# Kernel tuning notes

Hardware: AMD Instinct MI355X
Metric: run time of the kernel (lower is better)

## Reference

```python
import jax, jax.numpy as jnp
import numpy as np


def setup_inputs() -> dict:
    key = jax.random.key(0)
    ks = jax.random.split(key, 9)
    B, S, H, W = 4, 4096, 16, 16
    D = 256  # input_size == H*W == d_model
    sc = 1.0 / np.sqrt(D)
    return {
        "x": jax.random.normal(ks[0], (B, S, H, W), dtype=jnp.float32),
        "Wq": jax.random.normal(ks[1], (D, D), dtype=jnp.float32) * sc,
        "bq": jax.random.normal(ks[2], (D,), dtype=jnp.float32) * 0.01,
        "Wk": jax.random.normal(ks[3], (D, D), dtype=jnp.float32) * sc,
        "bk": jax.random.normal(ks[4], (D,), dtype=jnp.float32) * 0.01,
        "Wv": jax.random.normal(ks[5], (D, D), dtype=jnp.float32) * sc,
        "bv": jax.random.normal(ks[6], (D,), dtype=jnp.float32) * 0.01,
        "Wo": jax.random.normal(ks[7], (D, D), dtype=jnp.float32) * sc,
        "bo": jax.random.normal(ks[8], (D,), dtype=jnp.float32) * 0.01,
    }


def reference(x, Wq, bq, Wk, bk, Wv, bv, Wo, bo):
    B, S, H, W = x.shape
    xf = x.reshape(B, S, H * W)                      # [B, S, input_size]
    # nn.Linear: y = x @ W^T + b, weight shape [out, in]
    q = jax.nn.softplus(xf @ Wq.T + bq)              # [B, S, d]
    k = jax.nn.softplus(xf @ Wk.T + bk)              # [B, S, d]
    v = xf @ Wv.T + bv                               # [B, S, d]
    # naive ordering as in original: [B,S,S] scores, no softmax/normalization
    weight = jnp.einsum('bcd,bhd->bch', q, k)        # [B, S, S]
    result = jnp.einsum('bch,bhd->bcd', weight, v)   # [B, S, d]
    out = result @ Wo.T + bo                         # [B, S, input_size]
    return out.reshape(B, S, H, W)
```

## Files before the change

### kernel.cpp

```cpp
#include <hip/hip_runtime.h>
#include <hip/hip_bf16.h>
#include <math.h>

typedef __bf16 bf16_t;
typedef __bf16 bf16x8 __attribute__((ext_vector_type(8)));
typedef __bf16 bf16x4 __attribute__((ext_vector_type(4)));
typedef float  f32x4  __attribute__((ext_vector_type(4)));

#define NBATCH 4
#define SB     4096
#define BS     (NBATCH*SB)
#define DIM    256
#define NCHUNK 16


__device__ __forceinline__ float softplus_f(float x) {
  return fmaxf(x, 0.0f) + log1pf(__expf(-fabsf(x)));
}

__device__ __forceinline__ void gload_lds16(const void* g, void* l) {
  __builtin_amdgcn_global_load_lds(
      (const __attribute__((address_space(1))) void*)g,
      (__attribute__((address_space(3))) void*)l,
      16, 0, 0);
}

__device__ __forceinline__ void cvt4(const float* __restrict__ s,
                                     bf16_t* __restrict__ d, int qi) {
  const float4 v = *(const float4*)(s + (size_t)qi * 4);
  bf16x4 o;
  o[0] = (bf16_t)v.x; o[1] = (bf16_t)v.y; o[2] = (bf16_t)v.z; o[3] = (bf16_t)v.w;
  *(bf16x4*)(d + (size_t)qi * 4) = o;
}

__global__ void prep_all(const float* __restrict__ x,
                         const float* __restrict__ Wq,
                         const float* __restrict__ Wk,
                         const float* __restrict__ Wv,
                         const float* __restrict__ Wo,
                         const float* __restrict__ bv,
                         bf16_t* __restrict__ xb,
                         bf16_t* __restrict__ Wqb,
                         bf16_t* __restrict__ Wkb,
                         bf16_t* __restrict__ Wvob,
                         float* __restrict__ bvo) {
  if (blockIdx.x < 1024) {
    const int QX = BS * DIM / 4;
    const int QW = DIM * DIM / 4;
    const int total = QX + 2 * QW;
    for (int qi = blockIdx.x * blockDim.x + threadIdx.x; qi < total;
         qi += 1024 * blockDim.x) {
      if (qi < QX)           cvt4(x,  xb,  qi);
      else if (qi < QX + QW) cvt4(Wq, Wqb, qi - QX);
      else                   cvt4(Wk, Wkb, qi - QX - QW);
    }
  } else {
    const int j = blockIdx.x - 1024;
    const int t = threadIdx.x;
    float acc = 0.0f;
    for (int i = 0; i < DIM; ++i)
      acc = fmaf(Wo[j * DIM + i], Wv[i * DIM + t], acc);
    Wvob[(size_t)j * DIM + t] = (bf16_t)acc;
    if (t == 0) {
      float a = 0.0f;
      for (int i = 0; i < DIM; ++i) a = fmaf(Wo[j * DIM + i], bv[i], a);
      bvo[j] = a;
    }
  }
}

__device__ __forceinline__ void gemm128_core(
    const bf16_t* __restrict__ Abase,
    const bf16_t* __restrict__ Bbase,
    char* smem, int tid, f32x4 acc[4][4]) {
  const int lane = tid & 63;
  const int w = tid >> 6;
  const int wr = w & 1, wc = w >> 1;
  #pragma unroll
  for (int kk = 0; kk < 2; ++kk) {
    const char* asrc = (const char*)Abase + kk * 256;
    const char* bsrc = (const char*)Bbase + kk * 256;
    #pragma unroll
    for (int it = 0; it < 8; ++it) {
      const int L = it * 256 + tid;
      const int row = L >> 4;
      const int lch = (L & 15) ^ (row & 7);
      char* la = smem + (size_t)(it * 256 + w * 64) * 16;
      char* lb = la + 32768;
      gload_lds16(asrc + (size_t)row * 512 + lch * 16, la);
      gload_lds16(bsrc + (size_t)row * 512 + lch * 16, lb);
    }
    __syncthreads();
    #pragma unroll
    for (int ks = 0; ks < 4; ++ks) {
      const int kb = ks * 64 + ((lane >> 4) << 4);
      bf16x8 af[4], bg[4];
      #pragma unroll
      for (int mi = 0; mi < 4; ++mi) {
        const int row = wr * 64 + mi * 16 + (lane & 15);
        const int ch = (kb >> 4) ^ (row & 7);
        af[mi] = *(const bf16x8*)(smem + (size_t)row * 256 + ch * 16);
      }
      #pragma unroll
      for (int ni = 0; ni < 4; ++ni) {
        const int row = wc * 64 + ni * 16 + (lane & 15);
        const int ch = (kb >> 4) ^ (row & 7);
        bg[ni] = *(const bf16x8*)(smem + 32768 + (size_t)row * 256 + ch * 16);
      }
      #pragma unroll
      for (int mi = 0; mi < 4; ++mi)
        #pragma unroll
        for (int ni = 0; ni < 4; ++ni)
          acc[mi][ni] = __builtin_amdgcn_mfma_f32_16x16x32_bf16(
              af[mi], bg[ni], acc[mi][ni], 0, 0, 0);
    }
    __syncthreads();
  }
}

__global__ __launch_bounds__(256) void qkv_gemm(
    const bf16_t* __restrict__ xb,
    const bf16_t* __restrict__ Wqb,
    const bf16_t* __restrict__ Wkb,
    const bf16_t* __restrict__ Wvob,
    const float* __restrict__ bq,
    const float* __restrict__ bk,
    const float* __restrict__ bvo,
    bf16_t* __restrict__ qo,
    bf16_t* __restrict__ kT,
    bf16_t* __restrict__ vT) {
  __shared__ __align__(16) char smem[65536];
  const int mode = blockIdx.z;
  const int r0 = blockIdx.x * 128;
  const int c0 = blockIdx.y * 128;
  const bf16_t* W   = (mode == 0) ? Wqb : (mode == 1) ? Wkb : Wvob;
  const float* bias = (mode == 0) ? bq  : (mode == 1) ? bk  : bvo;
  const int tid = threadIdx.x;
  const int lane = tid & 63;
  const int w = tid >> 6;
  const int wr = w & 1, wc = w >> 1;

  f32x4 zero = {0.0f, 0.0f, 0.0f, 0.0f};
  f32x4 acc[4][4];
  #pragma unroll
  for (int i = 0; i < 4; ++i)
    #pragma unroll
    for (int j = 0; j < 4; ++j) acc[i][j] = zero;

  gemm128_core(xb + (size_t)r0 * DIM, W + (size_t)c0 * DIM, smem, tid, acc);

  const int batch = r0 >> 12;
  #pragma unroll
  for (int ni = 0; ni < 4; ++ni) {
    const int col = c0 + wc * 64 + ni * 16 + (lane & 15);
    const float bb = bias[col];
    #pragma unroll
    for (int mi = 0; mi < 4; ++mi) {
      const int srow = r0 + wr * 64 + mi * 16 + ((lane >> 4) << 2);
      f32x4 v = acc[mi][ni];
      float o0 = v[0] + bb, o1 = v[1] + bb, o2 = v[2] + bb, o3 = v[3] + bb;
      if (mode < 2) {
        o0 = softplus_f(o0); o1 = softplus_f(o1);
        o2 = softplus_f(o2); o3 = softplus_f(o3);
      }
      if (mode == 0) {
        qo[(size_t)(srow + 0) * DIM + col] = (bf16_t)o0;
        qo[(size_t)(srow + 1) * DIM + col] = (bf16_t)o1;
        qo[(size_t)(srow + 2) * DIM + col] = (bf16_t)o2;
        qo[(size_t)(srow + 3) * DIM + col] = (bf16_t)o3;
      } else {
        bf16_t* dst = (mode == 1) ? kT : vT;
        const int sin = srow & (SB - 1);
        bf16x4 p;
        p[0] = (bf16_t)o0; p[1] = (bf16_t)o1; p[2] = (bf16_t)o2; p[3] = (bf16_t)o3;
        *(bf16x4*)(dst + (size_t)batch * DIM * SB + (size_t)col * SB + sin) = p;
      }
    }
  }
}

__global__ __launch_bounds__(256) void m_gemm(
    const bf16_t* __restrict__ kT,
    const bf16_t* __restrict__ vT,
    float* __restrict__ MTp) {
  const int quad = blockIdx.x;
  const int sc   = blockIdx.y;
  const int b    = blockIdx.z;
  const int tid = threadIdx.x;
  const int lane = tid & 63;
  const int w = tid >> 6;
  const int wr = w & 1, wc = w >> 1;
  const int j0 = (quad & 1) * 128 + wr * 64;
  const int d0 = (quad >> 1) * 128 + wc * 64;
  const bf16_t* vb = vT + (size_t)b * DIM * SB;
  const bf16_t* kb = kT + (size_t)b * DIM * SB;

  f32x4 zero = {0.0f, 0.0f, 0.0f, 0.0f};
  f32x4 acc[4][4];
  #pragma unroll
  for (int i = 0; i < 4; ++i)
    #pragma unroll
    for (int j = 0; j < 4; ++j) acc[i][j] = zero;

  const int svec = sc * 256 + ((lane >> 4) << 3);
  #pragma unroll
  for (int it = 0; it < 8; ++it) {
    const int s = svec + it * 32;
    bf16x8 af[4], bg[4];
    #pragma unroll
    for (int mi = 0; mi < 4; ++mi)
      af[mi] = *(const bf16x8*)(vb + (size_t)(j0 + mi * 16 + (lane & 15)) * SB + s);
    #pragma unroll
    for (int ni = 0; ni < 4; ++ni)
      bg[ni] = *(const bf16x8*)(kb + (size_t)(d0 + ni * 16 + (lane & 15)) * SB + s);
    #pragma unroll
    for (int mi = 0; mi < 4; ++mi)
      #pragma unroll
      for (int ni = 0; ni < 4; ++ni)
        acc[mi][ni] = __builtin_amdgcn_mfma_f32_16x16x32_bf16(
            af[mi], bg[ni], acc[mi][ni], 0, 0, 0);
  }

  float* o = MTp + ((size_t)sc * NBATCH + b) * DIM * DIM;
  #pragma unroll
  for (int mi = 0; mi < 4; ++mi) {
    const int row = j0 + mi * 16 + ((lane >> 4) << 2);
    #pragma unroll
    for (int ni = 0; ni < 4; ++ni) {
      const int col = d0 + ni * 16 + (lane & 15);
      #pragma unroll
      for (int r = 0; r < 4; ++r)
        o[(size_t)(row + r) * DIM + col] = acc[mi][ni][r];
    }
  }
}

__global__ void reduce_nt(const float* __restrict__ MTp,
                          bf16_t* __restrict__ NTb) {
  const int qi = blockIdx.x * blockDim.x + threadIdx.x;
  f32x4 s = {0.0f, 0.0f, 0.0f, 0.0f};
  #pragma unroll
  for (int c = 0; c < NCHUNK; ++c) {
    const float4 v =
        *(const float4*)(MTp + (size_t)c * NBATCH * DIM * DIM + (size_t)qi * 4);
    s[0] += v.x; s[1] += v.y; s[2] += v.z; s[3] += v.w;
  }
  bf16x4 o;
  o[0] = (bf16_t)s[0]; o[1] = (bf16_t)s[1];
  o[2] = (bf16_t)s[2]; o[3] = (bf16_t)s[3];
  *(bf16x4*)(NTb + (size_t)qi * 4) = o;
}

__global__ __launch_bounds__(256) void out_gemm(
    const bf16_t* __restrict__ qo,
    const bf16_t* __restrict__ NTb,
    const float* __restrict__ bo,
    float* __restrict__ out) {
  __shared__ __align__(16) char smem[65536];
  const int r0 = blockIdx.x * 128;
  const int c0 = blockIdx.y * 128;
  const int batch = r0 >> 12;
  const int tid = threadIdx.x;
  const int lane = tid & 63;
  const int w = tid >> 6;
  const int wr = w & 1, wc = w >> 1;

  f32x4 zero = {0.0f, 0.0f, 0.0f, 0.0f};
  f32x4 acc[4][4];
  #pragma unroll
  for (int i = 0; i < 4; ++i)
    #pragma unroll
    for (int j = 0; j < 4; ++j) acc[i][j] = zero;

  gemm128_core(qo + (size_t)r0 * DIM,
               NTb + (size_t)batch * DIM * DIM + (size_t)c0 * DIM,
               smem, tid, acc);

  #pragma unroll
  for (int ni = 0; ni < 4; ++ni) {
    const int col = c0 + wc * 64 + ni * 16 + (lane & 15);
    const float bb = bo[col];
    #pragma unroll
    for (int mi = 0; mi < 4; ++mi) {
      const int srow = r0 + wr * 64 + mi * 16 + ((lane >> 4) << 2);
      f32x4 v = acc[mi][ni];
      #pragma unroll
      for (int r = 0; r < 4; ++r)
        out[(size_t)(srow + r) * DIM + col] = v[r] + bb;
    }
  }
}


extern "C" void kernel_launch(void* const* d_in, const int* in_sizes, int n_in,
                              void* d_out, int out_size, void* d_ws, size_t ws_size,
                              hipStream_t stream) {
  const float* x  = (const float*)d_in[0];
  const float* Wq = (const float*)d_in[1];
  const float* bq = (const float*)d_in[2];
  const float* Wk = (const float*)d_in[3];
  const float* bk = (const float*)d_in[4];
  const float* Wv = (const float*)d_in[5];
  const float* bv = (const float*)d_in[6];
  const float* Wo = (const float*)d_in[7];
  const float* bo = (const float*)d_in[8];
  float* out = (float*)d_out;

  char* ws = (char*)d_ws;
  bf16_t* xb   = (bf16_t*)(ws);
  bf16_t* qo   = (bf16_t*)(ws + 8388608);
  bf16_t* kT   = (bf16_t*)(ws + 16777216);
  bf16_t* vT   = (bf16_t*)(ws + 25165824);
  bf16_t* Wqb  = (bf16_t*)(ws + 33554432);
  bf16_t* Wkb  = (bf16_t*)(ws + 33685504);
  bf16_t* Wvob = (bf16_t*)(ws + 33816576);
  float*  bvo  = (float*)(ws + 33947648);
  bf16_t* NTb  = (bf16_t*)(ws + 33948672);
  float*  MTp  = (float*)(ws + 34472960);

  prep_all<<<1280, 256, 0, stream>>>(x, Wq, Wk, Wv, Wo, bv,
                                     xb, Wqb, Wkb, Wvob, bvo);
  qkv_gemm<<<dim3(128, 2, 3), 256, 0, stream>>>(xb, Wqb, Wkb, Wvob,
                                                bq, bk, bvo, qo, kT, vT);
  m_gemm<<<dim3(4, NCHUNK, 4), 256, 0, stream>>>(kT, vT, MTp);
  reduce_nt<<<256, 256, 0, stream>>>(MTp, NTb);
  out_gemm<<<dim3(128, 2), 256, 0, stream>>>(qo, NTb, bo, out);
}
```

Measured before the change: 149.6 us.

## Stage full weight panel in LDS and read activations directly from global

Replaces the two-step LDS-staged GEMM core with one that loads the whole 128x256 weight panel into LDS in a single step, with one barrier. The activation operand (x or q) is now read straight from global memory into registers for each MFMA step instead of going through LDS. This removes one LDS round-trip and several barriers per block. The cost is uncoalesced-ish 16-byte global loads of activations with no reuse across the two wave columns, and global latency sitting directly in the MFMA loop. The grid is also flattened from 3D to 2D so the mode index comes from blockIdx.y.

Result: slower. 175.3 us (+17.2%).

```diff
diff --git a/kernel.cpp b/kernel.cpp
--- a/kernel.cpp
+++ b/kernel.cpp
@@ -69,56 +69,54 @@
   }
 }
 
-__device__ __forceinline__ void gemm128_core(
-    const bf16_t* __restrict__ Abase,
-    const bf16_t* __restrict__ Bbase,
-    char* smem, int tid, f32x4 acc[4][4]) {
+
+__device__ __forceinline__ void stage_panel(const bf16_t* __restrict__ P,
+                                            char* smem, int tid) {
+  const int w = tid >> 6;
+  const char* src = (const char*)P;
+  #pragma unroll
+  for (int it = 0; it < 16; ++it) {
+    const int L = it * 256 + tid;
+    const int prow = L >> 5;
+    const int sch = (L & 31) ^ (prow & 7);
+    gload_lds16(src + (size_t)prow * 512 + sch * 16,
+                smem + (size_t)(it * 256 + w * 64) * 16);
+  }
+  __syncthreads();
+}
+
+__device__ __forceinline__ void panel_gemm_compute(
+    const bf16_t* __restrict__ Arow0,
+    const char* smem, int tid, f32x4 acc[4][4]) {
   const int lane = tid & 63;
   const int w = tid >> 6;
   const int wr = w & 1, wc = w >> 1;
-  #pragma unroll
-  for (int kk = 0; kk < 2; ++kk) {
-    const char* asrc = (const char*)Abase + kk * 256;
-    const char* bsrc = (const char*)Bbase + kk * 256;
-    #pragma unroll
-    for (int it = 0; it < 8; ++it) {
-      const int L = it * 256 + tid;
-      const int row = L >> 4;
-      const int lch = (L & 15) ^ (row & 7);
-      char* la = smem + (size_t)(it * 256 + w * 64) * 16;
-      char* lb = la + 32768;
-      gload_lds16(asrc + (size_t)row * 512 + lch * 16, la);
-      gload_lds16(bsrc + (size_t)row * 512 + lch * 16, lb);
-    }
-    __syncthreads();
-    #pragma unroll
-    for (int ks = 0; ks < 4; ++ks) {
-      const int kb = ks * 64 + ((lane >> 4) << 4);
-      bf16x8 af[4], bg[4];
+  const int arow_off = wr * 64 + (lane & 15);
+  const int brow_off = wc * 64 + (lane & 15);
+  const int kvec = (lane >> 4) << 3;
+  #pragma unroll
+  for (int ks = 0; ks < 8; ++ks) {
+    const int k = ks * 32 + kvec;
+    bf16x8 af[4], bg[4];
+    #pragma unroll
+    for (int mi = 0; mi < 4; ++mi)
+      af[mi] = *(const bf16x8*)(Arow0 + (size_t)(arow_off + mi * 16) * 256 + k);
+    #pragma unroll
+    for (int ni = 0; ni < 4; ++ni) {
+      const int prow = brow_off + ni * 16;
+      const int ch = (k >> 3) ^ (prow & 7);
+      bg[ni] = *(const bf16x8*)(smem + (size_t)prow * 512 + ch * 16);
+    }
+    #pragma unroll
+    for (int mi = 0; mi < 4; ++mi)
       #pragma unroll
-      for (int mi = 0; mi < 4; ++mi) {
-        const int row = wr * 64 + mi * 16 + (lane & 15);
-        const int ch = (kb >> 4) ^ (row & 7);
-        af[mi] = *(const bf16x8*)(smem + (size_t)row * 256 + ch * 16);
-      }
-      #pragma unroll
-      for (int ni = 0; ni < 4; ++ni) {
-        const int row = wc * 64 + ni * 16 + (lane & 15);
-        const int ch = (kb >> 4) ^ (row & 7);
-        bg[ni] = *(const bf16x8*)(smem + 32768 + (size_t)row * 256 + ch * 16);
-      }
-      #pragma unroll
-      for (int mi = 0; mi < 4; ++mi)
-        #pragma unroll
-        for (int ni = 0; ni < 4; ++ni)
-          acc[mi][ni] = __builtin_amdgcn_mfma_f32_16x16x32_bf16(
-              af[mi], bg[ni], acc[mi][ni], 0, 0, 0);
-    }
-    __syncthreads();
-  }
-}
-
-__global__ __launch_bounds__(256) void qkv_gemm(
+      for (int ni = 0; ni < 4; ++ni)
+        acc[mi][ni] = __builtin_amdgcn_mfma_f32_16x16x32_bf16(
+            af[mi], bg[ni], acc[mi][ni], 0, 0, 0);
+  }
+}
+
+__global__ __launch_bounds__(256) void proj_gemm(
     const bf16_t* __restrict__ xb,
     const bf16_t* __restrict__ Wqb,
     const bf16_t* __restrict__ Wkb,
@@ -130,9 +128,9 @@
     bf16_t* __restrict__ kT,
     bf16_t* __restrict__ vT) {
   __shared__ __align__(16) char smem[65536];
-  const int mode = blockIdx.z;
+  const int mode = blockIdx.y >> 1;
+  const int c0 = (blockIdx.y & 1) * 128;
   const int r0 = blockIdx.x * 128;
-  const int c0 = blockIdx.y * 128;
   const bf16_t* W   = (mode == 0) ? Wqb : (mode == 1) ? Wkb : Wvob;
   const float* bias = (mode == 0) ? bq  : (mode == 1) ? bk  : bvo;
   const int tid = threadIdx.x;
@@ -140,6 +138,8 @@
   const int w = tid >> 6;
   const int wr = w & 1, wc = w >> 1;
 
+  stage_panel(W + (size_t)c0 * DIM, smem, tid);
+
   f32x4 zero = {0.0f, 0.0f, 0.0f, 0.0f};
   f32x4 acc[4][4];
   #pragma unroll
@@ -147,7 +147,7 @@
     #pragma unroll
     for (int j = 0; j < 4; ++j) acc[i][j] = zero;
 
-  gemm128_core(xb + (size_t)r0 * DIM, W + (size_t)c0 * DIM, smem, tid, acc);
+  panel_gemm_compute(xb + (size_t)r0 * DIM, smem, tid, acc);
 
   const int batch = r0 >> 12;
   #pragma unroll
@@ -265,6 +265,8 @@
   const int w = tid >> 6;
   const int wr = w & 1, wc = w >> 1;
 
+  stage_panel(NTb + (size_t)batch * DIM * DIM + (size_t)c0 * DIM, smem, tid);
+
   f32x4 zero = {0.0f, 0.0f, 0.0f, 0.0f};
   f32x4 acc[4][4];
   #pragma unroll
@@ -272,9 +274,7 @@
     #pragma unroll
     for (int j = 0; j < 4; ++j) acc[i][j] = zero;
 
-  gemm128_core(qo + (size_t)r0 * DIM,
-               NTb + (size_t)batch * DIM * DIM + (size_t)c0 * DIM,
-               smem, tid, acc);
+  panel_gemm_compute(qo + (size_t)r0 * DIM, smem, tid, acc);
 
   #pragma unroll
   for (int ni = 0; ni < 4; ++ni) {
@@ -320,8 +320,8 @@
 
   prep_all<<<1280, 256, 0, stream>>>(x, Wq, Wk, Wv, Wo, bv,
                                      xb, Wqb, Wkb, Wvob, bvo);
-  qkv_gemm<<<dim3(128, 2, 3), 256, 0, stream>>>(xb, Wqb, Wkb, Wvob,
-                                                bq, bk, bvo, qo, kT, vT);
+  proj_gemm<<<dim3(128, 6), 256, 0, stream>>>(xb, Wqb, Wkb, Wvob,
+                                              bq, bk, bvo, qo, kT, vT);
   m_gemm<<<dim3(4, NCHUNK, 4), 256, 0, stream>>>(kT, vT, MTp);
   reduce_nt<<<256, 256, 0, stream>>>(MTp, NTb);
   out_gemm<<<dim3(128, 2), 256, 0, stream>>>(qo, NTb, bo, out);
```

## Fuse all stages into one cooperative persistent kernel with grid syncs

Applied to the files above, without the earlier changes.

Replaces five separate kernel launches with a single cooperative mega-kernel of 512 blocks that runs prep, QKV GEMM, the K^T V partial GEMM, the reduction and the output GEMM, separated by grid-wide syncs. The split-S chunking for the M GEMM changes from 16 chunks to 32 so that it fills the 512 blocks. The aim is to remove launch overhead and inter-kernel gaps. In exchange it adds grid-sync costs, gives uneven work distribution in some phases, doubles the partial-sum buffer, and keeps the old kernels as a fallback if the cooperative launch fails.

New measurement: 399.4 us. 167% more time.

```diff
diff --git a/kernel.cpp b/kernel.cpp
--- a/kernel.cpp
+++ b/kernel.cpp
@@ -1,6 +1,9 @@
 #include <hip/hip_runtime.h>
 #include <hip/hip_bf16.h>
+#include <hip/hip_cooperative_groups.h>
 #include <math.h>
+
+namespace cg = cooperative_groups;
 
 typedef __bf16 bf16_t;
 typedef __bf16 bf16x8 __attribute__((ext_vector_type(8)));
@@ -11,7 +14,6 @@
 #define SB     4096
 #define BS     (NBATCH*SB)
 #define DIM    256
-#define NCHUNK 16
 
 
 __device__ __forceinline__ float softplus_f(float x) {
@@ -31,42 +33,6 @@
   bf16x4 o;
   o[0] = (bf16_t)v.x; o[1] = (bf16_t)v.y; o[2] = (bf16_t)v.z; o[3] = (bf16_t)v.w;
   *(bf16x4*)(d + (size_t)qi * 4) = o;
-}
-
-__global__ void prep_all(const float* __restrict__ x,
-                         const float* __restrict__ Wq,
-                         const float* __restrict__ Wk,
-                         const float* __restrict__ Wv,
-                         const float* __restrict__ Wo,
-                         const float* __restrict__ bv,
-                         bf16_t* __restrict__ xb,
-                         bf16_t* __restrict__ Wqb,
-                         bf16_t* __restrict__ Wkb,
-                         bf16_t* __restrict__ Wvob,
-                         float* __restrict__ bvo) {
-  if (blockIdx.x < 1024) {
-    const int QX = BS * DIM / 4;
-    const int QW = DIM * DIM / 4;
-    const int total = QX + 2 * QW;
-    for (int qi = blockIdx.x * blockDim.x + threadIdx.x; qi < total;
-         qi += 1024 * blockDim.x) {
-      if (qi < QX)           cvt4(x,  xb,  qi);
-      else if (qi < QX + QW) cvt4(Wq, Wqb, qi - QX);
-      else                   cvt4(Wk, Wkb, qi - QX - QW);
-    }
-  } else {
-    const int j = blockIdx.x - 1024;
-    const int t = threadIdx.x;
-    float acc = 0.0f;
-    for (int i = 0; i < DIM; ++i)
-      acc = fmaf(Wo[j * DIM + i], Wv[i * DIM + t], acc);
-    Wvob[(size_t)j * DIM + t] = (bf16_t)acc;
-    if (t == 0) {
-      float a = 0.0f;
-      for (int i = 0; i < DIM; ++i) a = fmaf(Wo[j * DIM + i], bv[i], a);
-      bvo[j] = a;
-    }
-  }
 }
 
 __device__ __forceinline__ void gemm128_core(
@@ -118,24 +84,18 @@
   }
 }
 
-__global__ __launch_bounds__(256) void qkv_gemm(
+
+__device__ __forceinline__ void qkv_unit(
+    int mode, int r0, int c0, int tid, char* smem,
     const bf16_t* __restrict__ xb,
-    const bf16_t* __restrict__ Wqb,
-    const bf16_t* __restrict__ Wkb,
+    const bf16_t* __restrict__ Wqb, const bf16_t* __restrict__ Wkb,
     const bf16_t* __restrict__ Wvob,
-    const float* __restrict__ bq,
-    const float* __restrict__ bk,
+    const float* __restrict__ bq, const float* __restrict__ bk,
     const float* __restrict__ bvo,
-    bf16_t* __restrict__ qo,
-    bf16_t* __restrict__ kT,
+    bf16_t* __restrict__ qo, bf16_t* __restrict__ kT,
     bf16_t* __restrict__ vT) {
-  __shared__ __align__(16) char smem[65536];
-  const int mode = blockIdx.z;
-  const int r0 = blockIdx.x * 128;
-  const int c0 = blockIdx.y * 128;
   const bf16_t* W   = (mode == 0) ? Wqb : (mode == 1) ? Wkb : Wvob;
   const float* bias = (mode == 0) ? bq  : (mode == 1) ? bk  : bvo;
-  const int tid = threadIdx.x;
   const int lane = tid & 63;
   const int w = tid >> 6;
   const int wr = w & 1, wc = w >> 1;
@@ -179,14 +139,10 @@
   }
 }
 
-__global__ __launch_bounds__(256) void m_gemm(
-    const bf16_t* __restrict__ kT,
-    const bf16_t* __restrict__ vT,
+__device__ __forceinline__ void m_unit(
+    int quad, int sc, int b, int tid, int iters, int chunk_elems,
+    const bf16_t* __restrict__ kT, const bf16_t* __restrict__ vT,
     float* __restrict__ MTp) {
-  const int quad = blockIdx.x;
-  const int sc   = blockIdx.y;
-  const int b    = blockIdx.z;
-  const int tid = threadIdx.x;
   const int lane = tid & 63;
   const int w = tid >> 6;
   const int wr = w & 1, wc = w >> 1;
@@ -202,9 +158,8 @@
     #pragma unroll
     for (int j = 0; j < 4; ++j) acc[i][j] = zero;
 
-  const int svec = sc * 256 + ((lane >> 4) << 3);
-  #pragma unroll
-  for (int it = 0; it < 8; ++it) {
+  const int svec = sc * chunk_elems + ((lane >> 4) << 3);
+  for (int it = 0; it < iters; ++it) {
     const int s = svec + it * 32;
     bf16x8 af[4], bg[4];
     #pragma unroll
@@ -235,12 +190,11 @@
   }
 }
 
-__global__ void reduce_nt(const float* __restrict__ MTp,
-                          bf16_t* __restrict__ NTb) {
-  const int qi = blockIdx.x * blockDim.x + threadIdx.x;
+__device__ __forceinline__ void reduce_fn(int qi, int n,
+                                          const float* __restrict__ MTp,
+                                          bf16_t* __restrict__ NTb) {
   f32x4 s = {0.0f, 0.0f, 0.0f, 0.0f};
-  #pragma unroll
-  for (int c = 0; c < NCHUNK; ++c) {
+  for (int c = 0; c < n; ++c) {
     const float4 v =
         *(const float4*)(MTp + (size_t)c * NBATCH * DIM * DIM + (size_t)qi * 4);
     s[0] += v.x; s[1] += v.y; s[2] += v.z; s[3] += v.w;
@@ -251,16 +205,11 @@
   *(bf16x4*)(NTb + (size_t)qi * 4) = o;
 }
 
-__global__ __launch_bounds__(256) void out_gemm(
-    const bf16_t* __restrict__ qo,
-    const bf16_t* __restrict__ NTb,
-    const float* __restrict__ bo,
-    float* __restrict__ out) {
-  __shared__ __align__(16) char smem[65536];
-  const int r0 = blockIdx.x * 128;
-  const int c0 = blockIdx.y * 128;
+__device__ __forceinline__ void out_unit(
+    int r0, int c0, int tid, char* smem,
+    const bf16_t* __restrict__ qo, const bf16_t* __restrict__ NTb,
+    const float* __restrict__ bo, float* __restrict__ out) {
   const int batch = r0 >> 12;
-  const int tid = threadIdx.x;
   const int lane = tid & 63;
   const int w = tid >> 6;
   const int wr = w & 1, wc = w >> 1;
@@ -289,6 +238,126 @@
         out[(size_t)(srow + r) * DIM + col] = v[r] + bb;
     }
   }
+}
+
+__global__ __launch_bounds__(256) void mega_kernel(
+    const float* __restrict__ x,  const float* __restrict__ Wq,
+    const float* __restrict__ bq, const float* __restrict__ Wk,
+    const float* __restrict__ bk, const float* __restrict__ Wv,
+    const float* __restrict__ bv, const float* __restrict__ Wo,
+    const float* __restrict__ bo, float* __restrict__ out,
+    bf16_t* __restrict__ xb,  bf16_t* __restrict__ qo,
+    bf16_t* __restrict__ kT,  bf16_t* __restrict__ vT,
+    bf16_t* __restrict__ Wqb, bf16_t* __restrict__ Wkb,
+    bf16_t* __restrict__ Wvob, float* __restrict__ bvo,
+    bf16_t* __restrict__ NTb, float* __restrict__ MTp) {
+  cg::grid_group grid = cg::this_grid();
+  __shared__ __align__(16) char smem[65536];
+  const int bid = blockIdx.x;
+  const int tid = threadIdx.x;
+
+  if (bid < 256) {
+    const int QX = BS * DIM / 4, QW = DIM * DIM / 4;
+    for (int qi = bid * 256 + tid; qi < QX + 2 * QW; qi += 256 * 256) {
+      if (qi < QX)           cvt4(x,  xb,  qi);
+      else if (qi < QX + QW) cvt4(Wq, Wqb, qi - QX);
+      else                   cvt4(Wk, Wkb, qi - QX - QW);
+    }
+  } else {
+    const int j = bid - 256, t = tid;
+    float a = 0.0f;
+    for (int i = 0; i < DIM; ++i)
+      a = fmaf(Wo[j * DIM + i], Wv[i * DIM + t], a);
+    Wvob[(size_t)j * DIM + t] = (bf16_t)a;
+    if (t == 0) {
+      float s = 0.0f;
+      for (int i = 0; i < DIM; ++i) s = fmaf(Wo[j * DIM + i], bv[i], s);
+      bvo[j] = s;
+    }
+  }
+  grid.sync();
+
+  for (int u = bid; u < 768; u += 512) {
+    const int mode = u >> 8;
+    const int rest = u & 255;
+    qkv_unit(mode, (rest >> 1) * 128, (rest & 1) * 128, tid, smem,
+             xb, Wqb, Wkb, Wvob, bq, bk, bvo, qo, kT, vT);
+  }
+  grid.sync();
+
+  m_unit(bid >> 7, (bid >> 2) & 31, bid & 3, tid, 4, 128, kT, vT, MTp);
+  grid.sync();
+
+  {
+    const int qi = bid * 256 + tid;
+    if (qi < NBATCH * DIM * DIM / 4) reduce_fn(qi, 32, MTp, NTb);
+  }
+  grid.sync();
+
+  if (bid < 256)
+    out_unit((bid >> 1) * 128, (bid & 1) * 128, tid, smem, qo, NTb, bo, out);
+}
+
+
+__global__ void prep_fb(const float* __restrict__ x,
+                        const float* __restrict__ Wq,
+                        const float* __restrict__ Wk,
+                        const float* __restrict__ Wv,
+                        const float* __restrict__ Wo,
+                        const float* __restrict__ bv,
+                        bf16_t* __restrict__ xb, bf16_t* __restrict__ Wqb,
+                        bf16_t* __restrict__ Wkb, bf16_t* __restrict__ Wvob,
+                        float* __restrict__ bvo) {
+  if (blockIdx.x < 1024) {
+    const int QX = BS * DIM / 4, QW = DIM * DIM / 4;
+    for (int qi = blockIdx.x * blockDim.x + threadIdx.x; qi < QX + 2 * QW;
+         qi += 1024 * blockDim.x) {
+      if (qi < QX)           cvt4(x,  xb,  qi);
+      else if (qi < QX + QW) cvt4(Wq, Wqb, qi - QX);
+      else                   cvt4(Wk, Wkb, qi - QX - QW);
+    }
+  } else {
+    const int j = blockIdx.x - 1024, t = threadIdx.x;
+    float a = 0.0f;
+    for (int i = 0; i < DIM; ++i)
+      a = fmaf(Wo[j * DIM + i], Wv[i * DIM + t], a);
+    Wvob[(size_t)j * DIM + t] = (bf16_t)a;
+    if (t == 0) {
+      float s = 0.0f;
+      for (int i = 0; i < DIM; ++i) s = fmaf(Wo[j * DIM + i], bv[i], s);
+      bvo[j] = s;
+    }
+  }
+}
+
+__global__ __launch_bounds__(256) void qkv_fb(
+    const bf16_t* __restrict__ xb, const bf16_t* __restrict__ Wqb,
+    const bf16_t* __restrict__ Wkb, const bf16_t* __restrict__ Wvob,
+    const float* __restrict__ bq, const float* __restrict__ bk,
+    const float* __restrict__ bvo, bf16_t* __restrict__ qo,
+    bf16_t* __restrict__ kT, bf16_t* __restrict__ vT) {
+  __shared__ __align__(16) char smem[65536];
+  qkv_unit(blockIdx.z, blockIdx.x * 128, blockIdx.y * 128, threadIdx.x, smem,
+           xb, Wqb, Wkb, Wvob, bq, bk, bvo, qo, kT, vT);
+}
+
+__global__ __launch_bounds__(256) void m_fb(const bf16_t* __restrict__ kT,
+                                            const bf16_t* __restrict__ vT,
+                                            float* __restrict__ MTp) {
+  m_unit(blockIdx.x, blockIdx.y, blockIdx.z, threadIdx.x, 8, 256, kT, vT, MTp);
+}
+
+__global__ void reduce_fb(const float* __restrict__ MTp,
+                          bf16_t* __restrict__ NTb) {
+  reduce_fn(blockIdx.x * blockDim.x + threadIdx.x, 16, MTp, NTb);
+}
+
+__global__ __launch_bounds__(256) void out_fb(
+    const bf16_t* __restrict__ qo, const bf16_t* __restrict__ NTb,
+    const float* __restrict__ bo, float* __restrict__ out) {
+  __shared__ __align__(16) char smem[65536];
+  out_unit(blockIdx.x * 128, blockIdx.y * 128, threadIdx.x, smem,
+           qo, NTb, bo, out);
 }
 
 
@@ -318,11 +387,30 @@
   bf16_t* NTb  = (bf16_t*)(ws + 33948672);
   float*  MTp  = (float*)(ws + 34472960);
 
-  prep_all<<<1280, 256, 0, stream>>>(x, Wq, Wk, Wv, Wo, bv,
-                                     xb, Wqb, Wkb, Wvob, bvo);
-  qkv_gemm<<<dim3(128, 2, 3), 256, 0, stream>>>(xb, Wqb, Wkb, Wvob,
+  int dev = 0, coop = 0;
+  hipGetDevice(&dev);
+  hipDeviceGetAttribute(&coop, hipDeviceAttributeCooperativeLaunch, dev);
+
+  bool done = false;
+  if (coop) {
+    void* args[] = {(void*)&x,  (void*)&Wq, (void*)&bq, (void*)&Wk,
+                    (void*)&bk, (void*)&Wv, (void*)&bv, (void*)&Wo,
+                    (void*)&bo, (void*)&out,
+                    (void*)&xb, (void*)&qo, (void*)&kT, (void*)&vT,
+                    (void*)&Wqb, (void*)&Wkb, (void*)&Wvob, (void*)&bvo,
+                    (void*)&NTb, (void*)&MTp};
+    hipError_t e = hipLaunchCooperativeKernel((const void*)mega_kernel,
+                                              dim3(512), dim3(256),
+                                              args, 0, stream);
+    done = (e == hipSuccess);
+  }
+  if (!done) {
+    prep_fb<<<1280, 256, 0, stream>>>(x, Wq, Wk, Wv, Wo, bv,
+                                      xb, Wqb, Wkb, Wvob, bvo);
+    qkv_fb<<<dim3(128, 2, 3), 256, 0, stream>>>(xb, Wqb, Wkb, Wvob,
                                                 bq, bk, bvo, qo, kT, vT);
-  m_gemm<<<dim3(4, NCHUNK, 4), 256, 0, stream>>>(kT, vT, MTp);
-  reduce_nt<<<256, 256, 0, stream>>>(MTp, NTb);
-  out_gemm<<<dim3(128, 2), 256, 0, stream>>>(qo, NTb, bo, out);
-}
+    m_fb<<<dim3(4, 16, 4), 256, 0, stream>>>(kT, vT, MTp);
+    reduce_fb<<<256, 256, 0, stream>>>(MTp, NTb);
+    out_fb<<<dim3(128, 2), 256, 0, stream>>>(qo, NTb, bo, out);
+  }
+}
```
